# Kernel tuning notes

Hardware: AMD Instinct MI355X
Metric: run time of the kernel (lower is better)

## Reference

```python
import jax, jax.numpy as jnp
import numpy as np

NUM_EMBEDDINGS = 1024
EMBEDDING_DIM = 64
COMMITMENT_COST = 0.25


def setup_inputs() -> dict:
    key = jax.random.key(0)
    k_x, k_cb = jax.random.split(key)
    x = jax.random.normal(k_x, (16, EMBEDDING_DIM, 64, 64), dtype=jnp.float32)
    # nn.Embedding weight init: uniform(-1/K, 1/K)
    codebook = jax.random.uniform(
        k_cb, (NUM_EMBEDDINGS, EMBEDDING_DIM), dtype=jnp.float32,
        minval=-1.0 / NUM_EMBEDDINGS, maxval=1.0 / NUM_EMBEDDINGS)
    return {"x": x, "codebook": codebook}


def reference(x, codebook):
    sg = jax.lax.stop_gradient
    # NCHW -> NHWC
    inputs = jnp.transpose(x, (0, 2, 3, 1))  # [B,H,W,D]
    in_shape = inputs.shape
    flat = inputs.reshape(-1, EMBEDDING_DIM)  # [N,D]
    # squared L2 distances to each codebook entry: [N,K]
    distances = (jnp.sum(flat ** 2, axis=1, keepdims=True)
                 + jnp.sum(codebook ** 2, axis=1)
                 - 2.0 * jnp.matmul(flat, codebook.T))
    encoding_indices = jnp.argmin(distances, axis=1)  # [N]
    # one-hot matmul in the original == plain gather
    quantized = codebook[encoding_indices].reshape(in_shape)  # [B,H,W,D]
    e_latent_loss = jnp.mean((sg(quantized) - inputs) ** 2)
    q_latent_loss = jnp.mean((quantized - sg(inputs)) ** 2)
    loss = q_latent_loss + COMMITMENT_COST * e_latent_loss
    # straight-through estimator
    quantized = inputs + sg(quantized - inputs)
    quantized = jnp.transpose(quantized, (0, 3, 1, 2))  # NHWC -> NCHW
    return quantized, loss
```

## Files before the change

### kernel.cpp

```cpp
#include <hip/hip_runtime.h>

#define NPTS   65536
#define DIM    64
#define KCODES 1024
#define HW     4096
#define ROWP   72

typedef __attribute__((ext_vector_type(8))) short  short8;
typedef __attribute__((ext_vector_type(4))) float  floatx4;

__device__ __forceinline__ short f2bf(float f) {
    unsigned u = __builtin_bit_cast(unsigned, f);
    u = (u + 0x7FFFu + ((u >> 16) & 1u)) >> 16;
    return (short)u;
}
__device__ __forceinline__ float bf2f(short s) {
    unsigned u = ((unsigned)(unsigned short)s) << 16;
    return __builtin_bit_cast(float, u);
}

__global__ void vq_prep(const float* __restrict__ cb, short* __restrict__ cbbf,
                        float* __restrict__ cbn, float* __restrict__ loss_ptr) {
    int k = blockIdx.x * 256 + threadIdx.x;
    if (k == 0) *loss_ptr = 0.0f;
    if (k >= KCODES) return;
    const float* row = cb + (size_t)k * DIM;
    float ns = 0.0f;
    #pragma unroll
    for (int c = 0; c < 8; ++c) {
        short8 v;
        #pragma unroll
        for (int e = 0; e < 8; ++e) {
            short h = f2bf(row[c * 8 + e]);
            v[e] = h;
            float cf = bf2f(h);
            ns = fmaf(cf, cf, ns);
        }
        *(short8*)&cbbf[(size_t)k * DIM + c * 8] = v;
    }
    cbn[k] = -0.5f * ns;
}

__global__ __launch_bounds__(1024, 4) void vq_main(
    const float* __restrict__ x, const short* __restrict__ cbbf,
    const float* __restrict__ cbn, float* __restrict__ out,
    float* __restrict__ loss_ptr)
{
    __shared__ __align__(16) short s_cb[KCODES * ROWP];
    __shared__ float s_cbn[KCODES];
    __shared__ float s_part[4][256];
    __shared__ float s_red[16];

    const int tid  = threadIdx.x;
    const int lane = tid & 63;
    const int wave = tid >> 6;
    const int col  = lane & 15;
    const int quad = lane >> 4;
    const int pg   = wave & 3;
    const int kc   = wave >> 2;

    #pragma unroll
    for (int i = 0; i < 8; ++i) {
        int chunk = tid + 1024 * i;
        short8 v = *(const short8*)(cbbf + (size_t)chunk * 8);
        int code = chunk >> 3, part = chunk & 7;
        *(short8*)&s_cb[code * ROWP + part * 8] = v;
    }
    s_cbn[tid & 1023] = cbn[tid & 1023];

    const int p0 = blockIdx.x * 256;
    short8 afrag[4][2];
    #pragma unroll
    for (int p = 0; p < 4; ++p) {
        int n = p0 + pg * 64 + p * 16 + col;
        const float* bp = x + ((size_t)(n >> 12) << 18) + (n & 4095);
        #pragma unroll
        for (int kh = 0; kh < 2; ++kh) {
            int dbase = kh * 32 + quad * 8;
            short8 f;
            #pragma unroll
            for (int j = 0; j < 8; ++j)
                f[j] = f2bf(bp[(size_t)(dbase + j) * HW]);
            afrag[p][kh] = f;
        }
    }
    __syncthreads();

    float best[4][4];
    #pragma unroll
    for (int p = 0; p < 4; ++p)
        #pragma unroll
        for (int r = 0; r < 4; ++r) best[p][r] = -3.4e38f;

    #pragma unroll 4
    for (int t = 0; t < 16; ++t) {
        const int code = kc * 256 + t * 16 + col;
        const float initv = s_cbn[code];
        const unsigned idxv = (unsigned)code;
        const short* rp = &s_cb[code * ROWP];
        const short8 b0 = *(const short8*)(rp + quad * 8);
        const short8 b1 = *(const short8*)(rp + 32 + quad * 8);
        floatx4 cinit = {initv, initv, initv, initv};
        #pragma unroll
        for (int p = 0; p < 4; ++p) {
            floatx4 acc = __builtin_amdgcn_mfma_f32_16x16x32_bf16(afrag[p][0], b0, cinit, 0, 0, 0);
            acc = __builtin_amdgcn_mfma_f32_16x16x32_bf16(afrag[p][1], b1, acc, 0, 0, 0);
            #pragma unroll
            for (int r = 0; r < 4; ++r) {
                unsigned pb = (__builtin_bit_cast(unsigned, acc[r]) & 0xFFFFFC00u) | idxv;
                best[p][r] = fmaxf(best[p][r], __builtin_bit_cast(float, pb));
            }
        }
    }

    #pragma unroll
    for (int p = 0; p < 4; ++p)
        #pragma unroll
        for (int r = 0; r < 4; ++r) {
            float v = best[p][r];
            v = fmaxf(v, __shfl_xor(v, 1, 64));
            v = fmaxf(v, __shfl_xor(v, 2, 64));
            v = fmaxf(v, __shfl_xor(v, 4, 64));
            v = fmaxf(v, __shfl_xor(v, 8, 64));
            best[p][r] = v;
        }
    if (col == 0) {
        #pragma unroll
        for (int p = 0; p < 4; ++p)
            #pragma unroll
            for (int r = 0; r < 4; ++r)
                s_part[kc][pg * 64 + p * 16 + quad * 4 + r] = best[p][r];
    }
    __syncthreads();

    {
        int pt = tid & 255;
        int dq = tid >> 8;
        float m = fmaxf(fmaxf(s_part[0][pt], s_part[1][pt]),
                        fmaxf(s_part[2][pt], s_part[3][pt]));
        int idx = (int)(__builtin_bit_cast(unsigned, m) & 1023u);

        int n = p0 + pt;
        size_t base = ((size_t)(n >> 12) << 18) + (n & 4095);
        float* op = out + base;
        const float* xp = x + base;
        float lsum = 0.0f;
        #pragma unroll
        for (int j = 0; j < 4; ++j) {
            unsigned long long u = *(const unsigned long long*)&s_cb[idx * ROWP + dq * 16 + j * 4];
            #pragma unroll
            for (int e = 0; e < 4; ++e) {
                int d = dq * 16 + j * 4 + e;
                float c = bf2f((short)(u >> (16 * e)));
                float xv = xp[(size_t)d * HW];
                op[(size_t)d * HW] = c;
                float diff = xv - c;
                lsum = fmaf(diff, diff, lsum);
            }
        }
        #pragma unroll
        for (int off = 32; off > 0; off >>= 1)
            lsum += __shfl_down(lsum, off, 64);
        if (lane == 0) s_red[wave] = lsum;
    }
    __syncthreads();
    if (tid == 0) {
        float s = 0.0f;
        #pragma unroll
        for (int w = 0; w < 16; ++w) s += s_red[w];
        atomicAdd(loss_ptr, s * (1.25f / (float)((size_t)NPTS * DIM)));
    }
}

extern "C" void kernel_launch(void* const* d_in, const int* in_sizes, int n_in,
                              void* d_out, int out_size, void* d_ws, size_t ws_size,
                              hipStream_t stream) {
    const float* x  = (const float*)d_in[0];
    const float* cb = (const float*)d_in[1];
    float* out      = (float*)d_out;
    float* loss_ptr = out + (size_t)NPTS * DIM;

    short* cbbf = (short*)d_ws;
    float* cbn  = (float*)((char*)d_ws + KCODES * DIM * sizeof(short));

    vq_prep<<<KCODES / 256, 256, 0, stream>>>(cb, cbbf, cbn, loss_ptr);
    vq_main<<<NPTS / 256, 1024, 0, stream>>>(x, cbbf, cbn, out, loss_ptr);
}
```

Measured before the change: 90.49 us.

## Stream codebook through LDS in chunks and compute loss from distance

Shrinks blocks to 512 threads over 128 points and streams the bf16 codebook through a small LDS buffer in 8 chunks of 128 codes, instead of staging the whole 1024-code codebook per block. The goal is to cut LDS footprint and per-block staging so more blocks stay resident. The loss is now derived from the input norm computed during fragment load plus the winning max-distance value, so x is no longer re-read in the epilogue. The gather for the output reads the codebook from global memory. The costs are extra barriers per chunk, and a loss computed from the truncated, bf16-based distance that may differ slightly from the exact one.

```diff
diff --git a/kernel.cpp b/kernel.cpp
--- a/kernel.cpp
+++ b/kernel.cpp
@@ -4,6 +4,8 @@
 #define DIM    64
 #define KCODES 1024
 #define HW     4096
+#define CH     128
+#define NCH    8
 #define ROWP   72
 
 typedef __attribute__((ext_vector_type(8))) short  short8;
@@ -41,15 +43,16 @@
     cbn[k] = -0.5f * ns;
 }
 
-__global__ __launch_bounds__(1024, 4) void vq_main(
+__global__ __launch_bounds__(512, 4) void vq_main(
     const float* __restrict__ x, const short* __restrict__ cbbf,
     const float* __restrict__ cbn, float* __restrict__ out,
     float* __restrict__ loss_ptr)
 {
-    __shared__ __align__(16) short s_cb[KCODES * ROWP];
+    __shared__ __align__(16) short s_cb[CH * ROWP];
     __shared__ float s_cbn[KCODES];
-    __shared__ float s_part[4][256];
-    __shared__ float s_red[16];
+    __shared__ float s_part[2][128];
+    __shared__ float s_xn[128];
+    __shared__ float s_red[2];
 
     const int tid  = threadIdx.x;
     const int lane = tid & 63;
@@ -59,117 +62,122 @@
     const int pg   = wave & 3;
     const int kc   = wave >> 2;
 
+    const int pb = blockIdx.x * 128 + pg * 32;
+    short8 afrag[2][2];
+    float  xnorm[2];
     #pragma unroll
-    for (int i = 0; i < 8; ++i) {
-        int chunk = tid + 1024 * i;
-        short8 v = *(const short8*)(cbbf + (size_t)chunk * 8);
-        int code = chunk >> 3, part = chunk & 7;
-        *(short8*)&s_cb[code * ROWP + part * 8] = v;
-    }
-    s_cbn[tid & 1023] = cbn[tid & 1023];
-
-    const int p0 = blockIdx.x * 256;
-    short8 afrag[4][2];
-    #pragma unroll
-    for (int p = 0; p < 4; ++p) {
-        int n = p0 + pg * 64 + p * 16 + col;
+    for (int pt = 0; pt < 2; ++pt) {
+        int n = pb + pt * 16 + col;
         const float* bp = x + ((size_t)(n >> 12) << 18) + (n & 4095);
+        float ns = 0.0f;
         #pragma unroll
         for (int kh = 0; kh < 2; ++kh) {
-            int dbase = kh * 32 + quad * 8;
             short8 f;
             #pragma unroll
-            for (int j = 0; j < 8; ++j)
-                f[j] = f2bf(bp[(size_t)(dbase + j) * HW]);
-            afrag[p][kh] = f;
+            for (int j = 0; j < 8; ++j) {
+                float v = bp[(size_t)(kh * 32 + quad * 8 + j) * HW];
+                f[j] = f2bf(v);
+                ns = fmaf(v, v, ns);
+            }
+            afrag[pt][kh] = f;
         }
+        ns += __shfl_xor(ns, 16, 64);
+        ns += __shfl_xor(ns, 32, 64);
+        xnorm[pt] = ns;
     }
-    __syncthreads();
+    if (kc == 0 && quad == 0) {
+        s_xn[pg * 32 + col]      = xnorm[0];
+        s_xn[pg * 32 + 16 + col] = xnorm[1];
+    }
+    s_cbn[tid]       = cbn[tid];
+    s_cbn[tid + 512] = cbn[tid + 512];
 
-    float best[4][4];
+    float best[2][4];
     #pragma unroll
-    for (int p = 0; p < 4; ++p)
+    for (int pt = 0; pt < 2; ++pt)
         #pragma unroll
-        for (int r = 0; r < 4; ++r) best[p][r] = -3.4e38f;
+        for (int r = 0; r < 4; ++r) best[pt][r] = -3.4e38f;
 
-    #pragma unroll 4
-    for (int t = 0; t < 16; ++t) {
-        const int code = kc * 256 + t * 16 + col;
-        const float initv = s_cbn[code];
-        const unsigned idxv = (unsigned)code;
-        const short* rp = &s_cb[code * ROWP];
-        const short8 b0 = *(const short8*)(rp + quad * 8);
-        const short8 b1 = *(const short8*)(rp + 32 + quad * 8);
-        floatx4 cinit = {initv, initv, initv, initv};
+    for (int c = 0; c < NCH; ++c) {
+        __syncthreads();
         #pragma unroll
-        for (int p = 0; p < 4; ++p) {
-            floatx4 acc = __builtin_amdgcn_mfma_f32_16x16x32_bf16(afrag[p][0], b0, cinit, 0, 0, 0);
-            acc = __builtin_amdgcn_mfma_f32_16x16x32_bf16(afrag[p][1], b1, acc, 0, 0, 0);
+        for (int i = 0; i < 2; ++i) {
+            int idx = tid + 512 * i;
+            short8 v = *(const short8*)(cbbf + (size_t)c * (CH * DIM) + (size_t)idx * 8);
+            *(short8*)&s_cb[(idx >> 3) * ROWP + (idx & 7) * 8] = v;
+        }
+        __syncthreads();
+        #pragma unroll
+        for (int ct = 0; ct < 4; ++ct) {
+            int cc = kc * 64 + ct * 16 + col;
+            int gcode = c * CH + cc;
+            float initv = s_cbn[gcode];
+            unsigned idxv = (unsigned)gcode;
+            const short* rp = &s_cb[cc * ROWP + quad * 8];
+            short8 b0 = *(const short8*)rp;
+            short8 b1 = *(const short8*)(rp + 32);
+            floatx4 cinit = {initv, initv, initv, initv};
             #pragma unroll
-            for (int r = 0; r < 4; ++r) {
-                unsigned pb = (__builtin_bit_cast(unsigned, acc[r]) & 0xFFFFFC00u) | idxv;
-                best[p][r] = fmaxf(best[p][r], __builtin_bit_cast(float, pb));
+            for (int pt = 0; pt < 2; ++pt) {
+                floatx4 acc = __builtin_amdgcn_mfma_f32_16x16x32_bf16(afrag[pt][0], b0, cinit, 0, 0, 0);
+                acc = __builtin_amdgcn_mfma_f32_16x16x32_bf16(afrag[pt][1], b1, acc, 0, 0, 0);
+                #pragma unroll
+                for (int r = 0; r < 4; ++r) {
+                    unsigned pbits = (__builtin_bit_cast(unsigned, acc[r]) & 0xFFFFFC00u) | idxv;
+                    best[pt][r] = fmaxf(best[pt][r], __builtin_bit_cast(float, pbits));
+                }
             }
         }
     }
 
     #pragma unroll
-    for (int p = 0; p < 4; ++p)
+    for (int pt = 0; pt < 2; ++pt)
         #pragma unroll
         for (int r = 0; r < 4; ++r) {
-            float v = best[p][r];
+            float v = best[pt][r];
             v = fmaxf(v, __shfl_xor(v, 1, 64));
             v = fmaxf(v, __shfl_xor(v, 2, 64));
             v = fmaxf(v, __shfl_xor(v, 4, 64));
             v = fmaxf(v, __shfl_xor(v, 8, 64));
-            best[p][r] = v;
+            best[pt][r] = v;
         }
     if (col == 0) {
         #pragma unroll
-        for (int p = 0; p < 4; ++p)
+        for (int pt = 0; pt < 2; ++pt)
             #pragma unroll
             for (int r = 0; r < 4; ++r)
-                s_part[kc][pg * 64 + p * 16 + quad * 4 + r] = best[p][r];
+                s_part[kc][pg * 32 + pt * 16 + quad * 4 + r] = best[pt][r];
     }
     __syncthreads();
 
     {
-        int pt = tid & 255;
-        int dq = tid >> 8;
-        float m = fmaxf(fmaxf(s_part[0][pt], s_part[1][pt]),
-                        fmaxf(s_part[2][pt], s_part[3][pt]));
-        int idx = (int)(__builtin_bit_cast(unsigned, m) & 1023u);
-
-        int n = p0 + pt;
-        size_t base = ((size_t)(n >> 12) << 18) + (n & 4095);
-        float* op = out + base;
-        const float* xp = x + base;
-        float lsum = 0.0f;
+        int ptid = tid & 127;
+        int dq   = tid >> 7;
+        float m = fmaxf(s_part[0][ptid], s_part[1][ptid]);
+        unsigned mu = __builtin_bit_cast(unsigned, m);
+        int idx = (int)(mu & 1023u);
+        int n = blockIdx.x * 128 + ptid;
+        float* op = out + ((size_t)(n >> 12) << 18) + (n & 4095);
+        const short* crow = cbbf + (size_t)idx * DIM + dq * 16;
         #pragma unroll
-        for (int j = 0; j < 4; ++j) {
-            unsigned long long u = *(const unsigned long long*)&s_cb[idx * ROWP + dq * 16 + j * 4];
+        for (int j = 0; j < 2; ++j) {
+            short8 v = *(const short8*)(crow + j * 8);
             #pragma unroll
-            for (int e = 0; e < 4; ++e) {
-                int d = dq * 16 + j * 4 + e;
-                float c = bf2f((short)(u >> (16 * e)));
-                float xv = xp[(size_t)d * HW];
-                op[(size_t)d * HW] = c;
-                float diff = xv - c;
-                lsum = fmaf(diff, diff, lsum);
-            }
+            for (int e = 0; e < 8; ++e)
+                op[(size_t)(dq * 16 + j * 8 + e) * HW] = bf2f(v[e]);
         }
-        #pragma unroll
-        for (int off = 32; off > 0; off >>= 1)
-            lsum += __shfl_down(lsum, off, 64);
-        if (lane == 0) s_red[wave] = lsum;
+        if (dq == 0) {
+            float vtr = __builtin_bit_cast(float, mu & 0xFFFFFC00u);
+            float lp = s_xn[ptid] - 2.0f * vtr;
+            #pragma unroll
+            for (int off = 32; off > 0; off >>= 1)
+                lp += __shfl_down(lp, off, 64);
+            if (lane == 0) s_red[wave] = lp;
+        }
     }
     __syncthreads();
-    if (tid == 0) {
-        float s = 0.0f;
-        #pragma unroll
-        for (int w = 0; w < 16; ++w) s += s_red[w];
-        atomicAdd(loss_ptr, s * (1.25f / (float)((size_t)NPTS * DIM)));
-    }
+    if (tid == 0)
+        atomicAdd(loss_ptr, (s_red[0] + s_red[1]) * (1.25f / ((float)NPTS * DIM)));
 }
 
 extern "C" void kernel_launch(void* const* d_in, const int* in_sizes, int n_in,
@@ -184,5 +192,5 @@
     float* cbn  = (float*)((char*)d_ws + KCODES * DIM * sizeof(short));
 
     vq_prep<<<KCODES / 256, 256, 0, stream>>>(cb, cbbf, cbn, loss_ptr);
-    vq_main<<<NPTS / 256, 1024, 0, stream>>>(x, cbbf, cbn, out, loss_ptr);
+    vq_main<<<NPTS / 128, 512, 0, stream>>>(x, cbbf, cbn, out, loss_ptr);
 }
```

Measured after the change: 91.48 us. No clear change (+1.1%).
